# Optimization experiments

Hardware: AMD Instinct MI355X
Metric: run time of the kernel (lower is better)

The kernel has to match this reference:

```python
import jax, jax.numpy as jnp
import numpy as np

WD, WH, WW = 2, 7, 7          # window size (d, h, w)
N = WD * WH * WW              # 98 tokens per window
DIM = 768
NH = 24
HD = DIM // NH                # 32
SCALE = HD ** -0.5
NW = 64                       # windows per image
B = 4
B_ = B * NW                   # 256


def _relative_position_index():
    d, h, w = np.meshgrid(np.arange(WD), np.arange(WH), np.arange(WW), indexing='ij')
    coords = np.stack([d.ravel(), h.ravel(), w.ravel()])        # (3, N)
    rel = (coords[:, :, None] - coords[:, None, :]).transpose(1, 2, 0)  # (N, N, 3)
    rel = rel + np.array([WD - 1, WH - 1, WW - 1])
    rel = rel * np.array([(2 * WH - 1) * (2 * WW - 1), 2 * WW - 1, 1])
    return rel.sum(-1).astype(np.int32)                         # (N, N)


def setup_inputs() -> dict:
    key = jax.random.key(0)
    ks = jax.random.split(key, 5)
    table_rows = (2 * WD - 1) * (2 * WH - 1) * (2 * WW - 1)     # 507
    return {
        'x': jax.random.normal(ks[0], (B_, N, DIM), jnp.float32),
        'mask': jax.random.normal(ks[1], (NW, N, N), jnp.float32),
        'qkv_w': jax.random.normal(ks[2], (3 * DIM, DIM), jnp.float32) * 0.02,
        'qkv_b': jax.random.normal(ks[3], (3 * DIM,), jnp.float32) * 0.02,
        'rel_table': jax.random.normal(ks[4], (table_rows, NH), jnp.float32) * 0.02,
        'rel_index': jnp.asarray(_relative_position_index()),
    }


def reference(x, mask, qkv_w, qkv_b, rel_table, rel_index):
    Bs, n, c = x.shape
    # qkv linear; einops '(nH hD qkv)' => last dim factored as (nH, hD, 3)
    qkv = x @ qkv_w.T + qkv_b                                   # (Bs, N, 3C)
    qkv = qkv.reshape(Bs, n, NH, HD, 3)
    q, k, v = (jnp.moveaxis(qkv, -1, 0)                         # (3, Bs, N, nH, hD)
                  .transpose(0, 1, 3, 2, 4))                    # (3, Bs, nH, N, hD)
    attn = jnp.einsum('bhqd,bhkd->bhqk', q, k) * SCALE          # (Bs, nH, N, N)
    bias = rel_table[rel_index]                                 # (N, N, nH)
    attn = attn + bias.transpose(2, 0, 1)[None]                 # + (1, nH, N, N)
    # window mask add
    attn = attn.reshape(Bs // NW, NW, NH, n, n) + mask[None, :, None]
    attn = attn.reshape(Bs, NH, n, n)
    attn = jax.nn.softmax(attn, axis=-1)
    out = jnp.einsum('bhqk,bhkd->bhqd', attn, v)                # (Bs, nH, N, hD)
    return out.transpose(0, 2, 1, 3).reshape(Bs, n, c)          # (Bs, N, C)
```

## Files before the change

### kernel.cpp

```cpp
#include <hip/hip_runtime.h>
#include <hip/hip_bf16.h>
#include <stdint.h>


#define NTOK 98
#define MT 7
#define NPAD 112
#define DIMX 768
#define NHEAD 24
#define HDIM 32
#define NQKV 2304
#define BROWS 25088
#define SCALE 0.17677669529663689f
#define LOG2E 1.4426950408889634f
#define SCL2E (SCALE * LOG2E)
#define NN2 (NTOK * NTOK)
#define BMROW 112
#define BMSZ (BMROW * BMROW)

#if __has_builtin(__builtin_amdgcn_exp2f)
#define EXP2F(x) __builtin_amdgcn_exp2f(x)
#else
#define EXP2F(x) exp2f(x)
#endif

typedef __attribute__((ext_vector_type(8))) short short8;
typedef __attribute__((ext_vector_type(4))) short short4v;
typedef __attribute__((ext_vector_type(4))) float floatx4;

__device__ __forceinline__ short f2b(float f) {
    __hip_bfloat16 h = __float2bfloat16(f);
    return __builtin_bit_cast(short, h);
}
__device__ __forceinline__ float b2f(unsigned short s) {
    return __builtin_bit_cast(float, ((unsigned)s) << 16);
}

__device__ __forceinline__ void gload_lds16(const void* g, void* l) {
    __builtin_amdgcn_global_load_lds(
        (const __attribute__((address_space(1))) void*)g,
        (__attribute__((address_space(3))) void*)l, 16, 0, 0);
}

__global__ void convert_kernel(const float* __restrict__ src,
                               short* __restrict__ dst, int n4) {
    int i = blockIdx.x * 256 + threadIdx.x;
    int stride = gridDim.x * 256;
    for (; i < n4; i += stride) {
        float4 f = ((const float4*)src)[i];
        short4v s = { f2b(f.x), f2b(f.y), f2b(f.z), f2b(f.w) };
        ((short4v*)dst)[i] = s;
    }
}

__global__ void convert_w_perm(const float* __restrict__ w,
                               short* __restrict__ wb) {
    int i = blockIdx.x * 256 + threadIdx.x;
    if (i >= NQKV * 192) return;
    int cp = i / 192, k4 = i % 192;
    int s = cp / DIMX, rem = cp % DIMX;
    int orig = (rem >> 5) * 96 + (rem & 31) * 3 + s;
    float sc = (s == 0) ? SCL2E : 1.0f;
    float4 f = ((const float4*)(w + (size_t)orig * DIMX))[k4];
    short4v o = { f2b(f.x * sc), f2b(f.y * sc), f2b(f.z * sc), f2b(f.w * sc) };
    ((short4v*)(wb + (size_t)cp * DIMX))[k4] = o;
}

__global__ void bm_kernel(const float* __restrict__ rel_table,
                          const int* __restrict__ rel_index,
                          const float* __restrict__ mask,
                          short* __restrict__ bm) {
    int t = blockIdx.x * 256 + threadIdx.x;
    if (t >= 64 * NHEAD * BMSZ / 4) return;
    int wh = t / (BMSZ / 4);
    int r4 = t % (BMSZ / 4);
    int i = r4 / 28;
    int j0 = (r4 % 28) * 4;
    int h = wh % NHEAD, w = wh / NHEAD;
    short4v o;
    #pragma unroll
    for (int jj = 0; jj < 4; ++jj) {
        int j = j0 + jj;
        float val = -1e30f;
        if (i < NTOK && j < NTOK) {
            float bv = rel_table[(size_t)rel_index[i * NTOK + j] * NHEAD + h];
            float mv = mask[(size_t)w * NN2 + i * NTOK + j];
            val = (bv + mv) * LOG2E;
        }
        o[jj] = f2b(val);
    }
    *(short4v*)(bm + (size_t)wh * BMSZ + i * BMROW + j0) = o;
}

__global__ void bias_gather_kernel(const float* __restrict__ rel_table,
                                   const int* __restrict__ rel_index,
                                   float* __restrict__ bias_pre) {
    int t = blockIdx.x * 256 + threadIdx.x;
    if (t >= NHEAD * NN2) return;
    int h  = t / NN2;
    int ij = t % NN2;
    bias_pre[t] = rel_table[(size_t)rel_index[ij] * NHEAD + h];
}

__global__ void gemm_kernel(const short* __restrict__ xb,
                            const short* __restrict__ wb,
                            const float* __restrict__ qkv_b,
                            short* __restrict__ qkv) {
    __shared__ short At[128 * 64];
    __shared__ short Bt[128 * 64];
    const int tid  = threadIdx.x;
    const int lane = tid & 63;
    const int wv   = tid >> 6;
    const int wr   = wv >> 1, wc = wv & 1;
    const int l15  = lane & 15;
    const int l4   = lane >> 4;

    int bid = blockIdx.x;
    int swz = (bid & 7) * 441 + (bid >> 3);
    const int mtile = swz / 18;
    const int ntile = swz % 18;

    const short* aB = xb + (size_t)(mtile * 128) * DIMX;
    const short* bB = wb + (size_t)(ntile * 128) * DIMX;
    const int lrow = lane >> 3;
    const int lcol = (lane & 7) * 8;

    floatx4 acc[4][4];
    #pragma unroll
    for (int m = 0; m < 4; ++m)
        #pragma unroll
        for (int n = 0; n < 4; ++n) acc[m][n] = (floatx4){0.f, 0.f, 0.f, 0.f};

    for (int kb = 0; kb < 12; ++kb) {
        #pragma unroll
        for (int j = 0; j < 4; ++j) {
            int r = wv * 32 + j * 8;
            gload_lds16(aB + (size_t)(r + lrow) * DIMX + kb * 64 + lcol, &At[r * 64]);
            gload_lds16(bB + (size_t)(r + lrow) * DIMX + kb * 64 + lcol, &Bt[r * 64]);
        }
        __syncthreads();
        #pragma unroll
        for (int kh = 0; kh < 2; ++kh) {
            int k0 = kh * 32 + l4 * 8;
            short8 af[4], bfr[4];
            #pragma unroll
            for (int m = 0; m < 4; ++m)
                af[m] = *(const short8*)(&At[(wr * 64 + m * 16 + l15) * 64 + k0]);
            #pragma unroll
            for (int n = 0; n < 4; ++n)
                bfr[n] = *(const short8*)(&Bt[(wc * 64 + n * 16 + l15) * 64 + k0]);
            #pragma unroll
            for (int m = 0; m < 4; ++m)
                #pragma unroll
                for (int n = 0; n < 4; ++n)
                    acc[m][n] = __builtin_amdgcn_mfma_f32_16x16x32_bf16(
                        af[m], bfr[n], acc[m][n], 0, 0, 0);
        }
        __syncthreads();
    }

    #pragma unroll
    for (int n = 0; n < 4; ++n) {
        int col = ntile * 128 + wc * 64 + n * 16 + l15;
        int s = col / DIMX, rem = col % DIMX;
        int orig = (rem >> 5) * 96 + (rem & 31) * 3 + s;
        float bias = qkv_b[orig] * ((s == 0) ? SCL2E : 1.0f);
        #pragma unroll
        for (int m = 0; m < 4; ++m) {
            int row0 = mtile * 128 + wr * 64 + m * 16 + l4 * 4;
            #pragma unroll
            for (int r = 0; r < 4; ++r)
                qkv[(size_t)(row0 + r) * NQKV + col] = f2b(acc[m][n][r] + bias);
        }
    }
}

struct __align__(16) SMemC {
    short P[NPAD * 128];
    short q[NPAD * HDIM];
    short k[NPAD * HDIM];
    short vt[HDIM * 128];
};

__global__ __launch_bounds__(256, 3) void attn_kernel4(
    const short* __restrict__ qkv,
    const short* __restrict__ bm,
    float* __restrict__ out) {
    __shared__ SMemC sm;
    const int tid  = threadIdx.x;
    const int lane = tid & 63;
    const int wv   = tid >> 6;
    const int l15  = lane & 15;
    const int l4   = lane >> 4;
    int id = blockIdx.x;
    int nb = (id & 7) * 768 + (id >> 3);
    const int b = nb / NHEAD;
    const int h = nb % NHEAD;
    const short* qbase = qkv + (size_t)b * NTOK * NQKV;

    #pragma unroll
    for (int it = 0; it < 2; ++it) {
        int row0 = it * 64 + wv * 16;
        if (row0 < NTOK) {
            int row = row0 + (lane >> 2);
            int seg = (lane & 3) * 8;
            if (row < NTOK) {
                gload_lds16(qbase + (size_t)row * NQKV + h * HDIM + seg,
                            &sm.q[row0 * HDIM]);
                gload_lds16(qbase + (size_t)row * NQKV + DIMX + h * HDIM + seg,
                            &sm.k[row0 * HDIM]);
            }
        }
    }
    if (tid < 196) {
        int t = (tid >> 2) * 2, dh = tid & 3;
        const short* vp = qbase + (size_t)t * NQKV + 2 * DIMX + h * HDIM + dh * 8;
        short8 va = *(const short8*)vp;
        short8 vb = *(const short8*)(vp + NQKV);
        #pragma unroll
        for (int j = 0; j < 8; ++j) {
            int d = dh * 8 + j;
            int csw = t ^ ((d & 7) << 3);
            unsigned pk = ((unsigned)(unsigned short)vb[j] << 16) |
                          (unsigned)(unsigned short)va[j];
            *(unsigned*)(&sm.vt[d * 128 + csw]) = pk;
        }
    }
    if (tid < 112) {
        int a = tid / 56, r2 = (tid % 56) >> 2, seg = (tid & 3) * 8;
        short* dst = (a ? sm.k : sm.q) + (NTOK + r2) * HDIM + seg;
        *(uint4*)dst = (uint4){0u, 0u, 0u, 0u};
    }
    for (int t = tid; t < HDIM * 30; t += 256) {
        int d = t / 30, c = NTOK + t % 30;
        sm.vt[d * 128 + (c ^ ((d & 7) << 3))] = 0;
    }
    for (int t = tid; t < NPAD * 16; t += 256) {
        int r = t >> 4, c = 112 + (t & 15);
        sm.P[r * 128 + (c ^ ((r & 7) << 3))] = 0;
    }
    __syncthreads();

    int mt[2];
    mt[0] = wv;
    mt[1] = (wv + 4 < MT) ? (wv + 4) : wv;

    floatx4 sacc[2][7];
    #pragma unroll
    for (int i = 0; i < 2; ++i)
        #pragma unroll
        for (int j = 0; j < 7; ++j) sacc[i][j] = (floatx4){0.f, 0.f, 0.f, 0.f};
    {
        int k0 = l4 * 8;
        short8 bq[2];
        #pragma unroll
        for (int iq = 0; iq < 2; ++iq)
            bq[iq] = *(const short8*)(&sm.q[(mt[iq] * 16 + l15) * HDIM + k0]);
        #pragma unroll
        for (int kt = 0; kt < 7; ++kt) {
            short8 ak = *(const short8*)(&sm.k[(kt * 16 + l15) * HDIM + k0]);
            #pragma unroll
            for (int iq = 0; iq < 2; ++iq)
                sacc[iq][kt] = __builtin_amdgcn_mfma_f32_16x16x32_bf16(
                    ak, bq[iq], sacc[iq][kt], 0, 0, 0);
        }
    }

    const short* bmh = bm + ((size_t)(b & 63) * NHEAD + h) * BMSZ;
    const int swzp = (l15 & 7) << 3;

    #pragma unroll
    for (int iq = 0; iq < 2; ++iq) {
        int q = mt[iq] * 16 + l15;
        const short* bmq = bmh + q * BMROW + l4 * 4;
        float vv[7][4];
        #pragma unroll
        for (int kt = 0; kt < 7; ++kt) {
            short4v bm4 = *(const short4v*)(bmq + kt * 16);
            #pragma unroll
            for (int r = 0; r < 4; ++r)
                vv[kt][r] = sacc[iq][kt][r] + b2f((unsigned short)bm4[r]);
        }
        float mx = vv[0][0];
        #pragma unroll
        for (int kt = 0; kt < 7; ++kt)
            #pragma unroll
            for (int r = 0; r < 4; ++r) mx = fmaxf(mx, vv[kt][r]);
        mx = fmaxf(mx, __shfl_xor(mx, 16));
        mx = fmaxf(mx, __shfl_xor(mx, 32));
        float s = 0.f;
        #pragma unroll
        for (int kt = 0; kt < 7; ++kt)
            #pragma unroll
            for (int r = 0; r < 4; ++r) {
                float e = EXP2F(vv[kt][r] - mx);
                vv[kt][r] = e;
                s += e;
            }
        s += __shfl_xor(s, 16);
        s += __shfl_xor(s, 32);
        float inv = (q < NTOK) ? 1.f / s : 0.f;
        #pragma unroll
        for (int kt = 0; kt < 7; ++kt) {
            short4v pw = { f2b(vv[kt][0] * inv), f2b(vv[kt][1] * inv),
                           f2b(vv[kt][2] * inv), f2b(vv[kt][3] * inv) };
            *(short4v*)(&sm.P[q * 128 + ((kt * 16 + l4 * 4) ^ swzp)]) = pw;
        }
    }
    __syncthreads();

    floatx4 oacc[2][2];
    #pragma unroll
    for (int i = 0; i < 2; ++i)
        #pragma unroll
        for (int j = 0; j < 2; ++j) oacc[i][j] = (floatx4){0.f, 0.f, 0.f, 0.f};

    #pragma unroll
    for (int kt = 0; kt < 4; ++kt) {
        int kk = (kt * 32 + l4 * 8) ^ swzp;
        short8 ap[2];
        #pragma unroll
        for (int im = 0; im < 2; ++im)
            ap[im] = *(const short8*)(&sm.P[(mt[im] * 16 + l15) * 128 + kk]);
        #pragma unroll
        for (int nt = 0; nt < 2; ++nt) {
            short8 bv = *(const short8*)(&sm.vt[(nt * 16 + l15) * 128 + kk]);
            #pragma unroll
            for (int im = 0; im < 2; ++im)
                oacc[im][nt] = __builtin_amdgcn_mfma_f32_16x16x32_bf16(
                    ap[im], bv, oacc[im][nt], 0, 0, 0);
        }
    }

    float* ob = out + (size_t)b * NTOK * DIMX + h * HDIM;
    #pragma unroll
    for (int im = 0; im < 2; ++im)
        #pragma unroll
        for (int nt = 0; nt < 2; ++nt) {
            int dd = nt * 16 + l15;
            #pragma unroll
            for (int r = 0; r < 4; ++r) {
                int tok = mt[im] * 16 + l4 * 4 + r;
                if (tok < NTOK)
                    ob[(size_t)tok * DIMX + dd] = oacc[im][nt][r];
            }
        }
}

struct __align__(16) SMemF {
    union {
        struct {
            short xt[NPAD * 64];
            short wt[96 * 64];
        } p1;
        short P[NPAD * 128];
    } u;
    short q[NPAD * HDIM];
    short k[NPAD * HDIM];
    short vt[HDIM * 128];
};

__global__ __launch_bounds__(256, 3) void attn_fused(
    const float* __restrict__ x,
    const float* __restrict__ mask,
    const float* __restrict__ qkv_w,
    const float* __restrict__ qkv_b,
    const float* __restrict__ bias_pre,
    const float* __restrict__ rel_table,
    const int* __restrict__ rel_index,
    float* __restrict__ out) {
    __shared__ SMemF sm;
    const int tid  = threadIdx.x;
    const int lane = tid & 63;
    const int wv   = tid >> 6;
    const int l15  = lane & 15;
    const int l4   = lane >> 4;
    const int b = blockIdx.x / NHEAD;
    const int h = blockIdx.x % NHEAD;
    const float* xp = x + (size_t)b * NTOK * DIMX;
    const float* wp = qkv_w + (size_t)h * 96 * DIMX;
    int mt[2];
    mt[0] = wv;
    mt[1] = (wv + 4 < MT) ? (wv + 4) : wv;

    floatx4 acc[2][6];
    #pragma unroll
    for (int i = 0; i < 2; ++i)
        #pragma unroll
        for (int j = 0; j < 6; ++j) acc[i][j] = (floatx4){0.f, 0.f, 0.f, 0.f};

    for (int kb = 0; kb < 12; ++kb) {
        for (int t = tid; t < NTOK * 16; t += 256) {
            int row = t >> 4, c = t & 15;
            float4 f = *(const float4*)(xp + (size_t)row * DIMX + kb * 64 + c * 4);
            short4v s = { f2b(f.x), f2b(f.y), f2b(f.z), f2b(f.w) };
            *(short4v*)(&sm.u.p1.xt[row * 64 + c * 4]) = s;
        }
        for (int t = tid; t < 96 * 16; t += 256) {
            int row = t >> 4, c = t & 15;
            float4 f = *(const float4*)(wp + (size_t)row * DIMX + kb * 64 + c * 4);
            short4v s = { f2b(f.x), f2b(f.y), f2b(f.z), f2b(f.w) };
            *(short4v*)(&sm.u.p1.wt[row * 64 + c * 4]) = s;
        }
        if (tid < 14 * 8) {
            int row = 98 + (tid >> 3), c = tid & 7;
            uint4 z = {0u, 0u, 0u, 0u};
            *(uint4*)(&sm.u.p1.xt[row * 64 + c * 8]) = z;
        }
        __syncthreads();
        #pragma unroll
        for (int ks = 0; ks < 2; ++ks) {
            int k0 = ks * 32 + l4 * 8;
            short8 aM[2];
            #pragma unroll
            for (int im = 0; im < 2; ++im)
                aM[im] = *(const short8*)(&sm.u.p1.xt[(mt[im] * 16 + l15) * 64 + k0]);
            #pragma unroll
            for (int nt = 0; nt < 6; ++nt) {
                short8 bN = *(const short8*)(&sm.u.p1.wt[(nt * 16 + l15) * 64 + k0]);
                #pragma unroll
                for (int im = 0; im < 2; ++im)
                    acc[im][nt] = __builtin_amdgcn_mfma_f32_16x16x32_bf16(
                        aM[im], bN, acc[im][nt], 0, 0, 0);
            }
        }
        __syncthreads();
    }

    #pragma unroll
    for (int im = 0; im < 2; ++im)
        #pragma unroll
        for (int nt = 0; nt < 6; ++nt) {
            int col = nt * 16 + l15;
            int d = col / 3, s = col % 3;
            float bias = qkv_b[h * 96 + col];
            #pragma unroll
            for (int r = 0; r < 4; ++r) {
                int tok = mt[im] * 16 + l4 * 4 + r;
                short val = f2b(acc[im][nt][r] + bias);
                if (s == 0)      sm.q[tok * HDIM + d] = val;
                else if (s == 1) sm.k[tok * HDIM + d] = val;
                else             sm.vt[d * 128 + tok] = val;
            }
        }
    __syncthreads();
    for (int t = tid; t < HDIM * 30; t += 256) {
        int d = t / 30, c = 98 + t % 30;
        sm.vt[d * 128 + c] = 0;
    }
    for (int t = tid; t < NPAD * 16; t += 256) {
        int row = t >> 4, c = 112 + (t & 15);
        sm.u.P[row * 128 + c] = 0;
    }

    floatx4 sacc[2][7];
    #pragma unroll
    for (int i = 0; i < 2; ++i)
        #pragma unroll
        for (int j = 0; j < 7; ++j) sacc[i][j] = (floatx4){0.f, 0.f, 0.f, 0.f};
    {
        int k0 = l4 * 8;
        short8 aq[2];
        #pragma unroll
        for (int im = 0; im < 2; ++im)
            aq[im] = *(const short8*)(&sm.q[(mt[im] * 16 + l15) * HDIM + k0]);
        #pragma unroll
        for (int nt = 0; nt < 7; ++nt) {
            short8 bk = *(const short8*)(&sm.k[(nt * 16 + l15) * HDIM + k0]);
            #pragma unroll
            for (int im = 0; im < 2; ++im)
                sacc[im][nt] = __builtin_amdgcn_mfma_f32_16x16x32_bf16(
                    aq[im], bk, sacc[im][nt], 0, 0, 0);
        }
    }

    const float* biash = bias_pre ? (bias_pre + (size_t)h * NN2) : nullptr;
    const size_t moff = (size_t)(b & 63) * NN2;

    #pragma unroll
    for (int im = 0; im < 2; ++im)
        #pragma unroll
        for (int r = 0; r < 4; ++r) {
            int row = mt[im] * 16 + l4 * 4 + r;
            bool vrow = row < NTOK;
            float v[7];
            #pragma unroll
            for (int nt = 0; nt < 7; ++nt) {
                int j = nt * 16 + l15;
                bool vj = vrow && (j < NTOK);
                float bmv = 0.f;
                if (vj) {
                    float bias = biash ? biash[row * NTOK + j]
                        : rel_table[(size_t)rel_index[row * NTOK + j] * NHEAD + h];
                    bmv = bias + mask[moff + row * NTOK + j];
                }
                v[nt] = vj ? sacc[im][nt][r] * SCALE + bmv : -1e30f;
            }
            float mx = v[0];
            #pragma unroll
            for (int nt = 1; nt < 7; ++nt) mx = fmaxf(mx, v[nt]);
            #pragma unroll
            for (int off = 1; off < 16; off <<= 1) mx = fmaxf(mx, __shfl_xor(mx, off));
            float s = 0.f;
            #pragma unroll
            for (int nt = 0; nt < 7; ++nt) {
                float e = (v[nt] > -1e29f) ? __expf(v[nt] - mx) : 0.f;
                v[nt] = e;
                s += e;
            }
            #pragma unroll
            for (int off = 1; off < 16; off <<= 1) s += __shfl_xor(s, off);
            float inv = vrow ? 1.f / s : 0.f;
            #pragma unroll
            for (int nt = 0; nt < 7; ++nt)
                sm.u.P[row * 128 + nt * 16 + l15] = f2b(v[nt] * inv);
        }
    __syncthreads();

    floatx4 oacc[2][2];
    #pragma unroll
    for (int i = 0; i < 2; ++i)
        #pragma unroll
        for (int j = 0; j < 2; ++j) oacc[i][j] = (floatx4){0.f, 0.f, 0.f, 0.f};
    #pragma unroll
    for (int kt = 0; kt < 4; ++kt) {
        int kk = kt * 32 + l4 * 8;
        short8 ap[2];
        #pragma unroll
        for (int im = 0; im < 2; ++im)
            ap[im] = *(const short8*)(&sm.u.P[(mt[im] * 16 + l15) * 128 + kk]);
        #pragma unroll
        for (int nt = 0; nt < 2; ++nt) {
            short8 bv = *(const short8*)(&sm.vt[(nt * 16 + l15) * 128 + kk]);
            #pragma unroll
            for (int im = 0; im < 2; ++im)
                oacc[im][nt] = __builtin_amdgcn_mfma_f32_16x16x32_bf16(
                    ap[im], bv, oacc[im][nt], 0, 0, 0);
        }
    }
    float* ob = out + (size_t)b * NTOK * DIMX + h * HDIM;
    #pragma unroll
    for (int im = 0; im < 2; ++im)
        #pragma unroll
        for (int nt = 0; nt < 2; ++nt) {
            int dd = nt * 16 + l15;
            #pragma unroll
            for (int r = 0; r < 4; ++r) {
                int tok = mt[im] * 16 + l4 * 4 + r;
                if (tok < NTOK)
                    ob[(size_t)tok * DIMX + dd] = oacc[im][nt][r];
            }
        }
}

extern "C" void kernel_launch(void* const* d_in, const int* in_sizes, int n_in,
                              void* d_out, int out_size, void* d_ws, size_t ws_size,
                              hipStream_t stream) {
    const float* x = (const float*)d_in[0];
    const float* mask = (const float*)d_in[1];
    const float* qkv_w = (const float*)d_in[2];
    const float* qkv_b = (const float*)d_in[3];
    const float* rel_table = (const float*)d_in[4];
    const int* rel_index = (const int*)d_in[5];
    for (int i = 0; i < n_in; ++i) {
        switch (in_sizes[i]) {
            case 256 * NTOK * DIMX:  x         = (const float*)d_in[i]; break;
            case 64 * NN2:           mask      = (const float*)d_in[i]; break;
            case 3 * DIMX * DIMX:    qkv_w     = (const float*)d_in[i]; break;
            case 3 * DIMX:           qkv_b     = (const float*)d_in[i]; break;
            case 507 * NHEAD:        rel_table = (const float*)d_in[i]; break;
            case NN2:                rel_index = (const int*)d_in[i]; break;
            default: break;
        }
    }
    float* out = (float*)d_out;

    const size_t xb_bytes   = (size_t)BROWS * DIMX * 2;
    const size_t wb_bytes   = (size_t)NQKV * DIMX * 2;
    const size_t qkv_bytes  = (size_t)BROWS * NQKV * 2;
    const size_t total      = xb_bytes + wb_bytes + qkv_bytes;

    if (ws_size >= total) {
        short* xb  = (short*)d_ws;
        short* wb  = (short*)((char*)d_ws + xb_bytes);
        short* qkv = (short*)((char*)d_ws + xb_bytes + wb_bytes);
        short* bmp = (short*)d_ws;

        int nx4 = BROWS * DIMX / 4;
        convert_kernel<<<(nx4 + 255) / 256, 256, 0, stream>>>(x, xb, nx4);
        convert_w_perm<<<(NQKV * 192 + 255) / 256, 256, 0, stream>>>(qkv_w, wb);
        gemm_kernel<<<196 * 18, 256, 0, stream>>>(xb, wb, qkv_b, qkv);
        int nbm = 64 * NHEAD * BMSZ / 4;
        bm_kernel<<<(nbm + 255) / 256, 256, 0, stream>>>(
            rel_table, rel_index, mask, bmp);
        attn_kernel4<<<256 * NHEAD, 256, 0, stream>>>(qkv, bmp, out);
    } else {
        const size_t bias_bytes = (size_t)NHEAD * NN2 * sizeof(float);
        float* bias_pre = (ws_size >= bias_bytes) ? (float*)d_ws : nullptr;
        if (bias_pre) {
            int nb = NHEAD * NN2;
            bias_gather_kernel<<<(nb + 255) / 256, 256, 0, stream>>>(rel_table, rel_index, bias_pre);
        }
        attn_fused<<<256 * NHEAD, 256, 0, stream>>>(x, mask, qkv_w, qkv_b,
                                                    bias_pre, rel_table, rel_index, out);
    }
}
```

Measured before the change: 357.5 us.

## Fuse preprocessing kernels into one launch and swizzle GEMM LDS tiles

Merges the x conversion, weight permute/convert and bias-mask build into a single prep kernel that dispatches on block index. When there is enough workspace, the bias-mask buffer gets its own region so it can be built before the GEMM instead of overwriting the x buffer afterwards. The GEMM applies an XOR swizzle to the LDS column offsets on both load and read to reduce bank conflicts on fragment reads. This cuts kernel launches and serialization, at the cost of a larger workspace requirement and some branch divergence in the prep kernel.

Measured after the change: 347.2 us. 1.03x faster.

```diff
diff --git a/kernel.cpp b/kernel.cpp
--- a/kernel.cpp
+++ b/kernel.cpp
@@ -18,6 +18,10 @@
 #define BMROW 112
 #define BMSZ (BMROW * BMROW)
 
+#define NB_X 18816
+#define NB_W 1728
+#define NB_BM 18816
+
 #if __has_builtin(__builtin_amdgcn_exp2f)
 #define EXP2F(x) __builtin_amdgcn_exp2f(x)
 #else
@@ -42,36 +46,11 @@
         (__attribute__((address_space(3))) void*)l, 16, 0, 0);
 }
 
-__global__ void convert_kernel(const float* __restrict__ src,
-                               short* __restrict__ dst, int n4) {
-    int i = blockIdx.x * 256 + threadIdx.x;
-    int stride = gridDim.x * 256;
-    for (; i < n4; i += stride) {
-        float4 f = ((const float4*)src)[i];
-        short4v s = { f2b(f.x), f2b(f.y), f2b(f.z), f2b(f.w) };
-        ((short4v*)dst)[i] = s;
-    }
-}
-
-__global__ void convert_w_perm(const float* __restrict__ w,
-                               short* __restrict__ wb) {
-    int i = blockIdx.x * 256 + threadIdx.x;
-    if (i >= NQKV * 192) return;
-    int cp = i / 192, k4 = i % 192;
-    int s = cp / DIMX, rem = cp % DIMX;
-    int orig = (rem >> 5) * 96 + (rem & 31) * 3 + s;
-    float sc = (s == 0) ? SCL2E : 1.0f;
-    float4 f = ((const float4*)(w + (size_t)orig * DIMX))[k4];
-    short4v o = { f2b(f.x * sc), f2b(f.y * sc), f2b(f.z * sc), f2b(f.w * sc) };
-    ((short4v*)(wb + (size_t)cp * DIMX))[k4] = o;
-}
-
-__global__ void bm_kernel(const float* __restrict__ rel_table,
-                          const int* __restrict__ rel_index,
-                          const float* __restrict__ mask,
-                          short* __restrict__ bm) {
-    int t = blockIdx.x * 256 + threadIdx.x;
-    if (t >= 64 * NHEAD * BMSZ / 4) return;
+__device__ __forceinline__ void bm_body(int t,
+                                        const float* __restrict__ rel_table,
+                                        const int* __restrict__ rel_index,
+                                        const float* __restrict__ mask,
+                                        short* __restrict__ bm) {
     int wh = t / (BMSZ / 4);
     int r4 = t % (BMSZ / 4);
     int i = r4 / 28;
@@ -90,6 +69,44 @@
         o[jj] = f2b(val);
     }
     *(short4v*)(bm + (size_t)wh * BMSZ + i * BMROW + j0) = o;
+}
+
+__global__ void prep_kernel(const float* __restrict__ x,
+                            const float* __restrict__ w,
+                            const float* __restrict__ rel_table,
+                            const int* __restrict__ rel_index,
+                            const float* __restrict__ mask,
+                            short* __restrict__ xb,
+                            short* __restrict__ wb,
+                            short* __restrict__ bm) {
+    int bid = blockIdx.x;
+    if (bid < NB_X) {
+        int i = bid * 256 + threadIdx.x;
+        float4 f = ((const float4*)x)[i];
+        short4v s = { f2b(f.x), f2b(f.y), f2b(f.z), f2b(f.w) };
+        ((short4v*)xb)[i] = s;
+    } else if (bid < NB_X + NB_W) {
+        int i = (bid - NB_X) * 256 + threadIdx.x;
+        int cp = i / 192, k4 = i % 192;
+        int s = cp / DIMX, rem = cp % DIMX;
+        int orig = (rem >> 5) * 96 + (rem & 31) * 3 + s;
+        float sc = (s == 0) ? SCL2E : 1.0f;
+        float4 f = ((const float4*)(w + (size_t)orig * DIMX))[k4];
+        short4v o = { f2b(f.x * sc), f2b(f.y * sc), f2b(f.z * sc), f2b(f.w * sc) };
+        ((short4v*)(wb + (size_t)cp * DIMX))[k4] = o;
+    } else {
+        int t = (bid - NB_X - NB_W) * 256 + threadIdx.x;
+        bm_body(t, rel_table, rel_index, mask, bm);
+    }
+}
+
+__global__ void bm_kernel(const float* __restrict__ rel_table,
+                          const int* __restrict__ rel_index,
+                          const float* __restrict__ mask,
+                          short* __restrict__ bm) {
+    int t = blockIdx.x * 256 + threadIdx.x;
+    if (t >= 64 * NHEAD * BMSZ / 4) return;
+    bm_body(t, rel_table, rel_index, mask, bm);
 }
 
 __global__ void bias_gather_kernel(const float* __restrict__ rel_table,
@@ -123,7 +140,8 @@
     const short* aB = xb + (size_t)(mtile * 128) * DIMX;
     const short* bB = wb + (size_t)(ntile * 128) * DIMX;
     const int lrow = lane >> 3;
-    const int lcol = (lane & 7) * 8;
+    const int lcs  = (((lane & 7) ^ lrow) * 8);
+    const int sa   = (l15 & 7) << 3;
 
     floatx4 acc[4][4];
     #pragma unroll
@@ -135,20 +153,21 @@
         #pragma unroll
         for (int j = 0; j < 4; ++j) {
             int r = wv * 32 + j * 8;
-            gload_lds16(aB + (size_t)(r + lrow) * DIMX + kb * 64 + lcol, &At[r * 64]);
-            gload_lds16(bB + (size_t)(r + lrow) * DIMX + kb * 64 + lcol, &Bt[r * 64]);
+            gload_lds16(aB + (size_t)(r + lrow) * DIMX + kb * 64 + lcs, &At[r * 64]);
+            gload_lds16(bB + (size_t)(r + lrow) * DIMX + kb * 64 + lcs, &Bt[r * 64]);
         }
         __syncthreads();
         #pragma unroll
         for (int kh = 0; kh < 2; ++kh) {
             int k0 = kh * 32 + l4 * 8;
+            int k0s = k0 ^ sa;
             short8 af[4], bfr[4];
             #pragma unroll
             for (int m = 0; m < 4; ++m)
-                af[m] = *(const short8*)(&At[(wr * 64 + m * 16 + l15) * 64 + k0]);
+                af[m] = *(const short8*)(&At[(wr * 64 + m * 16 + l15) * 64 + k0s]);
             #pragma unroll
             for (int n = 0; n < 4; ++n)
-                bfr[n] = *(const short8*)(&Bt[(wc * 64 + n * 16 + l15) * 64 + k0]);
+                bfr[n] = *(const short8*)(&Bt[(wc * 64 + n * 16 + l15) * 64 + k0s]);
             #pragma unroll
             for (int m = 0; m < 4; ++m)
                 #pragma unroll
@@ -578,22 +597,30 @@
     const size_t xb_bytes   = (size_t)BROWS * DIMX * 2;
     const size_t wb_bytes   = (size_t)NQKV * DIMX * 2;
     const size_t qkv_bytes  = (size_t)BROWS * NQKV * 2;
+    const size_t bm_bytes   = (size_t)64 * NHEAD * BMSZ * 2;
     const size_t total      = xb_bytes + wb_bytes + qkv_bytes;
 
     if (ws_size >= total) {
         short* xb  = (short*)d_ws;
         short* wb  = (short*)((char*)d_ws + xb_bytes);
         short* qkv = (short*)((char*)d_ws + xb_bytes + wb_bytes);
-        short* bmp = (short*)d_ws;
-
-        int nx4 = BROWS * DIMX / 4;
-        convert_kernel<<<(nx4 + 255) / 256, 256, 0, stream>>>(x, xb, nx4);
-        convert_w_perm<<<(NQKV * 192 + 255) / 256, 256, 0, stream>>>(qkv_w, wb);
-        gemm_kernel<<<196 * 18, 256, 0, stream>>>(xb, wb, qkv_b, qkv);
-        int nbm = 64 * NHEAD * BMSZ / 4;
-        bm_kernel<<<(nbm + 255) / 256, 256, 0, stream>>>(
-            rel_table, rel_index, mask, bmp);
-        attn_kernel4<<<256 * NHEAD, 256, 0, stream>>>(qkv, bmp, out);
+
+        if (ws_size >= total + bm_bytes) {
+            short* bmp = (short*)((char*)d_ws + total);
+            prep_kernel<<<NB_X + NB_W + NB_BM, 256, 0, stream>>>(
+                x, qkv_w, rel_table, rel_index, mask, xb, wb, bmp);
+            gemm_kernel<<<196 * 18, 256, 0, stream>>>(xb, wb, qkv_b, qkv);
+            attn_kernel4<<<256 * NHEAD, 256, 0, stream>>>(qkv, bmp, out);
+        } else {
+            short* bmp = (short*)d_ws;
+            prep_kernel<<<NB_X + NB_W, 256, 0, stream>>>(
+                x, qkv_w, rel_table, rel_index, mask, xb, wb, nullptr);
+            gemm_kernel<<<196 * 18, 256, 0, stream>>>(xb, wb, qkv_b, qkv);
+            int nbm = 64 * NHEAD * BMSZ / 4;
+            bm_kernel<<<(nbm + 255) / 256, 256, 0, stream>>>(
+                rel_table, rel_index, mask, bmp);
+            attn_kernel4<<<256 * NHEAD, 256, 0, stream>>>(qkv, bmp, out);
+        }
     } else {
         const size_t bias_bytes = (size_t)NHEAD * NN2 * sizeof(float);
         float* bias_pre = (ws_size >= bias_bytes) ? (float*)d_ws : nullptr;
```
